# Kernel tuning notes

Measured on AMD Instinct MI355X. Metric: run time of the kernel, lower is better.

The kernel has to match this reference:

```python
import jax, jax.numpy as jnp
import numpy as np

B, T, N, E, H, L, K = 2, 32, 256, 1024, 16, 2, 256
MAXLEN = 512  # RelativeMultiheadAttention max_seq_len default
SCALES = (1, 2, 4)
TAU = 1.0


def setup_inputs() -> dict:
    key = jax.random.key(0)
    ks = jax.random.split(key, 9)
    s = 0.02
    A = 2 * L  # [layer0-spatial, layer0-temporal, layer1-spatial, layer1-temporal]
    return {
        "x": jax.random.normal(ks[0], (B, T, N, E), jnp.float32),
        "attn_wq": jax.random.normal(ks[1], (A, E, E), jnp.float32) * s,
        "attn_bq": jnp.zeros((A, E), jnp.float32),
        "attn_wk": jax.random.normal(ks[2], (A, E, E), jnp.float32) * s,
        "attn_bk": jnp.zeros((A, E), jnp.float32),
        "attn_wv": jax.random.normal(ks[3], (A, E, E), jnp.float32) * s,
        "attn_bv": jnp.zeros((A, E), jnp.float32),
        "attn_wd": jax.random.normal(ks[4], (A, E, E), jnp.float32) * s,
        "attn_bd": jnp.zeros((A, E), jnp.float32),
        "rel_bias": jax.random.normal(ks[5], (A, 2 * MAXLEN - 1, H), jnp.float32) * s,
        "sel_w": jax.random.normal(ks[6], (E, K), jnp.float32) * s,
        "sel_b": jnp.zeros((K,), jnp.float32),
    }


def _rel_attn(x, wq, bq, wk, bk, wv, bv, wd, bd, rb):
    # x: [Bx, S, E]; rb: [2*MAXLEN-1, H]
    Bx, S, _ = x.shape
    D = E // H
    q = (x @ wq + bq).reshape(Bx, S, H, D)
    k = (x @ wk + bk).reshape(Bx, S, H, D)
    v = (x @ wv + bv).reshape(Bx, S, H, D)
    scores = jnp.einsum('bshd,bthd->bhst', q, k) / jnp.sqrt(jnp.asarray(D, x.dtype))
    pos = jnp.arange(S)
    idx = pos[None, :] - pos[:, None] + (MAXLEN - 1)  # [S, S]
    bias = rb[idx]  # [S, S, H] gathered relative-position bias
    scores = scores + bias.transpose(2, 0, 1)[None]
    w = jax.nn.softmax(scores, axis=-1)
    ctx = jnp.einsum('bhst,bthd->bshd', w, v).reshape(Bx, S, E)
    return ctx @ wd + bd


def reference(x, attn_wq, attn_bq, attn_wk, attn_bk, attn_wv, attn_bv,
              attn_wd, attn_bd, rel_bias, sel_w, sel_b):
    h = x
    for l in range(L):
        # spatial attention over tokens within each frame
        i = 2 * l
        hs = h.reshape(B * T, N, E)
        hs = _rel_attn(hs, attn_wq[i], attn_bq[i], attn_wk[i], attn_bk[i],
                       attn_wv[i], attn_bv[i], attn_wd[i], attn_bd[i], rel_bias[i])
        # temporal attention across frames per spatial location
        j = 2 * l + 1
        ht = hs.reshape(B, T, N, E).transpose(0, 2, 1, 3).reshape(B * N, T, E)
        ht = _rel_attn(ht, attn_wq[j], attn_bq[j], attn_wk[j], attn_bk[j],
                       attn_wv[j], attn_bv[j], attn_wd[j], attn_bd[j], rel_bias[j])
        h = ht.reshape(B, N, T, E).transpose(0, 2, 1, 3)
    # DifferentiableTokenSelection: softmax-weighted pooling into K tokens
    flat = h.reshape(B, T * N, E)
    sc = flat @ sel_w + sel_b  # [B, T*N, K]
    wts = jax.nn.softmax(sc / TAU, axis=1)
    sel = jnp.einsum('bmk,bme->bke', wts, flat)  # [B, K, E]
    # multi-scale average pooling (kernel==stride==scale), concat along tokens
    outs = [sel.reshape(B, K // s, s, E).mean(axis=2) for s in SCALES]
    return jnp.concatenate(outs, axis=1)  # [B, K + K//2 + K//4, E]
```

## Files before the change

kernel.cpp:

```cpp
#include <hip/hip_runtime.h>
#include <stdint.h>


using f16x8 = __attribute__((ext_vector_type(8))) _Float16;
using f16x4 = __attribute__((ext_vector_type(4))) _Float16;
using f32x4 = __attribute__((ext_vector_type(4))) float;

__device__ __forceinline__ int tmap_dev(int m) {
    int bx = m >> 5;
    int s  = m & 31;
    int b  = bx >> 8;
    int n  = bx & 255;
    return (((b << 5) + s) << 8) + n;
}

__device__ __forceinline__ void load16(const _Float16* g, _Float16* l)
{
    __builtin_amdgcn_global_load_lds(
        (const __attribute__((address_space(1))) unsigned int*)g,
        (__attribute__((address_space(3))) unsigned int*)l,
        16, 0, 0);
}

__device__ __forceinline__ void split_f16(float v, _Float16& h, _Float16& l)
{
    h = (_Float16)v;
    l = (_Float16)(v - (float)h);
}

__global__ __launch_bounds__(256)
void conv_act(const float* __restrict__ src, _Float16* __restrict__ dh,
              _Float16* __restrict__ dl, int m_off)
{
    int idx = blockIdx.x * 256 + threadIdx.x;
    int e = idx << 3;
    int ml = e >> 10, col = e & 1023;
    const float* s = src + (size_t)(m_off + ml) * 1024 + col;
    float4 a = *(const float4*)s;
    float4 b = *(const float4*)(s + 4);
    float vv[8] = {a.x, a.y, a.z, a.w, b.x, b.y, b.z, b.w};
    f16x8 vh, vl;
    #pragma unroll
    for (int r = 0; r < 8; r++) {
        _Float16 h, l;
        split_f16(vv[r], h, l);
        vh[r] = h; vl[r] = l;
    }
    *(f16x8*)(dh + (size_t)ml * 1024 + col) = vh;
    *(f16x8*)(dl + (size_t)ml * 1024 + col) = vl;
}

__global__ __launch_bounds__(256)
void conv_wT(const float* __restrict__ W, _Float16* __restrict__ Th,
             _Float16* __restrict__ Tl, int ncols)
{
    __shared__ float Ls[64][65];
    const int n0 = blockIdx.x * 64, k0 = blockIdx.y * 64;
    const int t = threadIdx.x;
    const int kk = t >> 4, nn = (t & 15) << 2;
    #pragma unroll
    for (int i = 0; i < 4; i++) {
        float4 v = *(const float4*)(W + (size_t)(k0 + kk + 16 * i) * ncols + n0 + nn);
        Ls[kk + 16 * i][nn + 0] = v.x; Ls[kk + 16 * i][nn + 1] = v.y;
        Ls[kk + 16 * i][nn + 2] = v.z; Ls[kk + 16 * i][nn + 3] = v.w;
    }
    __syncthreads();
    const int nl = t >> 4, kc = (t & 15) << 2;
    #pragma unroll
    for (int i = 0; i < 4; i++) {
        int n = nl + 16 * i;
        f16x4 hh, ll;
        #pragma unroll
        for (int c = 0; c < 4; c++) {
            _Float16 h, l;
            split_f16(Ls[kc + c][n], h, l);
            hh[c] = h; ll[c] = l;
        }
        *(f16x4*)(Th + (size_t)(n0 + n) * 1024 + k0 + kc) = hh;
        *(f16x4*)(Tl + (size_t)(n0 + n) * 1024 + k0 + kc) = ll;
    }
}

template<int EPI>
__device__ __forceinline__ void gemm_core(
    const _Float16* __restrict__ Ah, const _Float16* __restrict__ Al,
    const _Float16* __restrict__ Wh, const _Float16* __restrict__ Wl,
    const float* __restrict__ bias,
    float* __restrict__ C, _Float16* __restrict__ Ch, _Float16* __restrict__ Cl,
    int ldc, int map_in, int m_off_in, int map_out, int m_off_out,
    int n0, int m0)
{
    __shared__ uint32_t smem_u[8512];
    _Float16* smem = (_Float16*)smem_u;
    _Float16* sAh = smem;
    _Float16* sAl = smem + 4096;
    _Float16* sBh = smem + 8192;
    _Float16* sBl = smem + 12288;

    const int tid = threadIdx.x;
    const int lane = tid & 63;
    const int wv = tid >> 6;
    const int fm = (wv >> 1) << 6;
    const int fn = (wv & 1) << 6;
    const int lm = lane & 15, lq = lane >> 4;

    f32x4 acc[4][4] = {};

    const int srow = tid >> 2;
    const int skc  = (tid & 3) << 3;
    const int gm0 = m_off_in + m0 + srow;
    const int gm1 = gm0 + 64;
    const int r0 = map_in ? tmap_dev(gm0) : gm0;
    const int r1 = map_in ? tmap_dev(gm1) : gm1;
    const _Float16* gAh0 = Ah + (size_t)r0 * 1024 + skc;
    const _Float16* gAh1 = Ah + (size_t)r1 * 1024 + skc;
    const _Float16* gAl0 = Al + (size_t)r0 * 1024 + skc;
    const _Float16* gAl1 = Al + (size_t)r1 * 1024 + skc;
    const _Float16* gB0 = Wh + (size_t)(n0 + srow) * 1024 + skc;
    const _Float16* gB1 = Wl + (size_t)(n0 + srow) * 1024 + skc;
    const int lo = tid << 3;

    for (int k0 = 0; k0 < 1024; k0 += 32) {
        load16(gAh0 + k0, sAh + lo);
        load16(gAh1 + k0, sAh + lo + 2048);
        load16(gAl0 + k0, sAl + lo);
        load16(gAl1 + k0, sAl + lo + 2048);
        load16(gB0 + k0,         sBh + lo);
        load16(gB0 + k0 + 65536, sBh + lo + 2048);
        load16(gB1 + k0,         sBl + lo);
        load16(gB1 + k0 + 65536, sBl + lo + 2048);
        __syncthreads();

        f16x8 ah[4], al[4], bh[4], bl[4];
        #pragma unroll
        for (int i = 0; i < 4; i++) {
            int ra = (fm + i * 16 + lm) * 32 + lq * 8;
            ah[i] = *(const f16x8*)(sAh + ra);
            al[i] = *(const f16x8*)(sAl + ra);
            int rb_ = (fn + i * 16 + lm) * 32 + lq * 8;
            bh[i] = *(const f16x8*)(sBh + rb_);
            bl[i] = *(const f16x8*)(sBl + rb_);
        }
        #pragma unroll
        for (int i = 0; i < 4; i++)
            #pragma unroll
            for (int j = 0; j < 4; j++) {
                acc[i][j] = __builtin_amdgcn_mfma_f32_16x16x32_f16(ah[i], bh[j], acc[i][j], 0, 0, 0);
                acc[i][j] = __builtin_amdgcn_mfma_f32_16x16x32_f16(ah[i], bl[j], acc[i][j], 0, 0, 0);
                acc[i][j] = __builtin_amdgcn_mfma_f32_16x16x32_f16(al[i], bh[j], acc[i][j], 0, 0, 0);
            }
        __syncthreads();
    }

    if (EPI == 0) {
        #pragma unroll
        for (int j = 0; j < 4; j++) {
            int n = n0 + fn + j * 16 + lm;
            float bb = bias[n];
            #pragma unroll
            for (int i = 0; i < 4; i++) {
                #pragma unroll
                for (int r = 0; r < 4; r++) {
                    int gm = m_off_out + m0 + fm + i * 16 + lq * 4 + r;
                    int row = map_out ? tmap_dev(gm) : gm;
                    C[(size_t)row * ldc + n] = acc[i][j][r] + bb;
                }
            }
        }
    }
}

__global__ __launch_bounds__(256, 2)
void gemm_f16s_f32(const _Float16* __restrict__ Ah, const _Float16* __restrict__ Al,
                   int map_in, int m_off_in,
                   const _Float16* __restrict__ Wh, const _Float16* __restrict__ Wl,
                   const float* __restrict__ bias, float* __restrict__ C, int ldc,
                   int map_out, int m_off_out)
{
    gemm_core<0>(Ah, Al, Wh, Wl, bias, C, nullptr, nullptr, ldc,
                 map_in, m_off_in, map_out, m_off_out,
                 blockIdx.x * 128, blockIdx.y * 128);
}

template<int EPI>
__device__ __forceinline__ void gemm256_core(
    uint32_t* __restrict__ smem_u,
    const _Float16* __restrict__ Ah, const _Float16* __restrict__ Al,
    const _Float16* __restrict__ Wh, const _Float16* __restrict__ Wl,
    const float* __restrict__ bias,
    _Float16* __restrict__ Ch, _Float16* __restrict__ Cl,
    int map_in, int m_off_in, int map_out, int m_off_out,
    int n0, int m0)
{
    _Float16* S = (_Float16*)smem_u;
    const int tid  = threadIdx.x;
    const int lane = tid & 63;
    const int wv = tid >> 6;
    const int wm = wv >> 1;
    const int fm = wm << 6;
    const int fn = (wv & 1) << 6;
    const int lm = lane & 15, lq = lane >> 4;
    const int ko = ((lq ^ ((lm >> 1) & 3)) << 3);

    f32x4 acc[4][4] = {};

    const int srow = tid >> 2;
    const int scol = (((tid & 3) ^ ((tid >> 3) & 3)) << 3);
    const int gm0 = m_off_in + m0 + srow;
    const int gm1 = gm0 + 128;
    const int r0 = map_in ? tmap_dev(gm0) : gm0;
    const int r1 = map_in ? tmap_dev(gm1) : gm1;
    const _Float16* gAh0 = Ah + (size_t)r0 * 1024 + scol;
    const _Float16* gAh1 = Ah + (size_t)r1 * 1024 + scol;
    const _Float16* gAl0 = Al + (size_t)r0 * 1024 + scol;
    const _Float16* gAl1 = Al + (size_t)r1 * 1024 + scol;
    const _Float16* gBh  = Wh + (size_t)(n0 + srow) * 1024 + scol;
    const _Float16* gBl  = Wl + (size_t)(n0 + srow) * 1024 + scol;
    const int lo = tid << 3;

    auto stage = [&](int t, int b) {
        const int k0 = t << 5;
        _Float16* d = S + b * 24576;
        load16(gAh0 + k0, d + lo);
        load16(gAh1 + k0, d + 4096  + lo);
        load16(gAl0 + k0, d + 8192  + lo);
        load16(gAl1 + k0, d + 12288 + lo);
        load16(gBh  + k0, d + 16384 + lo);
        load16(gBl  + k0, d + 20480 + lo);
    };

    auto ldfrags = [&](const _Float16* c,
                       f16x8 (&xah)[4], f16x8 (&xal)[4],
                       f16x8 (&xbh)[4], f16x8 (&xbl)[4]) {
        #pragma unroll
        for (int i = 0; i < 4; i++) {
            int ra = (fm + i * 16 + lm) * 32 + ko;
            xah[i] = *(const f16x8*)(c + ra);
            xal[i] = *(const f16x8*)(c + 8192 + ra);
            int rb = (fn + i * 16 + lm) * 32 + ko;
            xbh[i] = *(const f16x8*)(c + 16384 + rb);
            xbl[i] = *(const f16x8*)(c + 20480 + rb);
        }
    };

    f16x8 ahA[4], alA[4], bhA[4], blA[4];
    f16x8 ahB[4], alB[4], bhB[4], blB[4];

    auto kstep = [&](int t, int nxtbuf, int stagebuf,
                     f16x8 (&cah)[4], f16x8 (&cal)[4],
                     f16x8 (&cbh)[4], f16x8 (&cbl)[4],
                     f16x8 (&nah)[4], f16x8 (&nal)[4],
                     f16x8 (&nbh)[4], f16x8 (&nbl)[4],
                     bool prefetch, bool dostage) {
        if (prefetch) ldfrags(S + nxtbuf * 24576, nah, nal, nbh, nbl);
        if (dostage) stage(t + 2, stagebuf);
        __builtin_amdgcn_sched_barrier(0);
        __builtin_amdgcn_s_setprio(1);
        #pragma unroll
        for (int i = 0; i < 4; i++)
            #pragma unroll
            for (int j = 0; j < 4; j++) {
                acc[i][j] = __builtin_amdgcn_mfma_f32_16x16x32_f16(cah[i], cbh[j], acc[i][j], 0, 0, 0);
                acc[i][j] = __builtin_amdgcn_mfma_f32_16x16x32_f16(cah[i], cbl[j], acc[i][j], 0, 0, 0);
                acc[i][j] = __builtin_amdgcn_mfma_f32_16x16x32_f16(cal[i], cbh[j], acc[i][j], 0, 0, 0);
            }
        __builtin_amdgcn_s_setprio(0);
        asm volatile("s_waitcnt vmcnt(0)" ::: "memory");
        __builtin_amdgcn_s_barrier();
    };

    stage(0, 0);
    stage(1, 1);
    asm volatile("s_waitcnt vmcnt(0)" ::: "memory");
    __builtin_amdgcn_s_barrier();
    ldfrags(S, ahA, alA, bhA, blA);

    #pragma unroll 1
    for (int tt = 0; tt < 30; tt += 6) {
        kstep(tt + 0, 1, 2, ahA, alA, bhA, blA, ahB, alB, bhB, blB, true, true);
        kstep(tt + 1, 2, 0, ahB, alB, bhB, blB, ahA, alA, bhA, blA, true, true);
        kstep(tt + 2, 0, 1, ahA, alA, bhA, blA, ahB, alB, bhB, blB, true, true);
        kstep(tt + 3, 1, 2, ahB, alB, bhB, blB, ahA, alA, bhA, blA, true, true);
        kstep(tt + 4, 2, 0, ahA, alA, bhA, blA, ahB, alB, bhB, blB, true, true);
        kstep(tt + 5, 0, 1, ahB, alB, bhB, blB, ahA, alA, bhA, blA, true, true);
    }
    kstep(30, 1, 0, ahA, alA, bhA, blA, ahB, alB, bhB, blB, true,  false);
    kstep(31, 0, 0, ahB, alB, bhB, blB, ahA, alA, bhA, blA, false, false);

    if (EPI == 1) {
        #pragma unroll 1
        for (int q = 0; q < 4; q++) {
            __syncthreads();
            if (wm == q) {
                #pragma unroll
                for (int j = 0; j < 4; j++) {
                    int ncol = fn + j * 16 + lm;
                    float bb = bias[n0 + ncol];
                    #pragma unroll
                    for (int i = 0; i < 4; i++) {
                        #pragma unroll
                        for (int r = 0; r < 4; r++) {
                            float v = acc[i][j][r] + bb;
                            _Float16 h, l;
                            split_f16(v, h, l);
                            uint32_t ph = (uint32_t)__builtin_bit_cast(unsigned short, h);
                            uint32_t pl = (uint32_t)__builtin_bit_cast(unsigned short, l);
                            smem_u[(i * 16 + lq * 4 + r) * 132 + ncol] = ph | (pl << 16);
                        }
                    }
                }
            }
            __syncthreads();
            #pragma unroll
            for (int g = 0; g < 2; g++) {
                int u = tid + g * 512;
                int rl = u >> 4;
                int c8 = (u & 15) << 3;
                uint32_t p[8];
                #pragma unroll
                for (int x = 0; x < 8; x++) p[x] = smem_u[rl * 132 + c8 + x];
                f16x8 hh, ll;
                #pragma unroll
                for (int x = 0; x < 8; x++) {
                    hh[x] = __builtin_bit_cast(_Float16, (unsigned short)(p[x] & 0xffff));
                    ll[x] = __builtin_bit_cast(_Float16, (unsigned short)(p[x] >> 16));
                }
                int gm = m_off_out + m0 + q * 64 + rl;
                int row = map_out ? tmap_dev(gm) : gm;
                *(f16x8*)(Ch + (size_t)row * 1024 + n0 + c8) = hh;
                *(f16x8*)(Cl + (size_t)row * 1024 + n0 + c8) = ll;
            }
        }
    } else {
        #pragma unroll 1
        for (int q = 0; q < 4; q++) {
            __syncthreads();
            if (wm == q) {
                #pragma unroll
                for (int j = 0; j < 4; j++) {
                    int ncol = fn + j * 16 + lm;
                    float bb = bias[n0 + ncol];
                    #pragma unroll
                    for (int i = 0; i < 4; i++) {
                        #pragma unroll
                        for (int r = 0; r < 4; r++) {
                            float v = acc[i][j][r] + bb;
                            _Float16 h, l;
                            split_f16(v, h, l);
                            uint32_t ph = (uint32_t)__builtin_bit_cast(unsigned short, h);
                            uint32_t pl = (uint32_t)__builtin_bit_cast(unsigned short, l);
                            smem_u[(i * 16 + lq * 4 + r) * 129 + ncol] = ph | (pl << 16);
                        }
                    }
                }
            }
            __syncthreads();
            #pragma unroll
            for (int g = 0; g < 4; g++) {
                int u = tid + g * 512;
                int nn = u >> 4;
                int mg = (u & 15) << 2;
                uint32_t p0 = smem_u[(mg + 0) * 129 + nn];
                uint32_t p1 = smem_u[(mg + 1) * 129 + nn];
                uint32_t p2 = smem_u[(mg + 2) * 129 + nn];
                uint32_t p3 = smem_u[(mg + 3) * 129 + nn];
                f16x4 hh, ll;
                hh[0] = __builtin_bit_cast(_Float16, (unsigned short)(p0 & 0xffff));
                hh[1] = __builtin_bit_cast(_Float16, (unsigned short)(p1 & 0xffff));
                hh[2] = __builtin_bit_cast(_Float16, (unsigned short)(p2 & 0xffff));
                hh[3] = __builtin_bit_cast(_Float16, (unsigned short)(p3 & 0xffff));
                ll[0] = __builtin_bit_cast(_Float16, (unsigned short)(p0 >> 16));
                ll[1] = __builtin_bit_cast(_Float16, (unsigned short)(p1 >> 16));
                ll[2] = __builtin_bit_cast(_Float16, (unsigned short)(p2 >> 16));
                ll[3] = __builtin_bit_cast(_Float16, (unsigned short)(p3 >> 16));
                size_t off = (size_t)(n0 + nn) * 8192 + (m0 + q * 64 + mg);
                *(f16x4*)(Ch + off) = hh;
                *(f16x4*)(Cl + off) = ll;
            }
        }
    }
}

__global__ __launch_bounds__(512, 2)
void gemm_qkv256(const _Float16* __restrict__ Ah, const _Float16* __restrict__ Al,
                 int map_in, int m_off_in,
                 const _Float16* __restrict__ WTh, const _Float16* __restrict__ WTl,
                 const float* __restrict__ bq, const float* __restrict__ bk,
                 const float* __restrict__ bv,
                 _Float16* __restrict__ Qh, _Float16* __restrict__ Ql,
                 _Float16* __restrict__ Kh, _Float16* __restrict__ Kl,
                 _Float16* __restrict__ VTh, _Float16* __restrict__ VTl)
{
    __shared__ uint32_t smem_u[36864];
    const int bid = blockIdx.x;
    const int wg = (bid & 7) * 96 + (bid >> 3);
    const int z = wg >> 8;
    const int rem = wg & 255;
    const int m0 = (rem >> 3) << 8;
    const int n0 = (rem & 7) << 7;
    const _Float16* wh = WTh + (size_t)z * 1048576;
    const _Float16* wl = WTl + (size_t)z * 1048576;
    if (z < 2) {
        const float* bb = (z == 0) ? bq : bk;
        _Float16* oh = (z == 0) ? Qh : Kh;
        _Float16* ol = (z == 0) ? Ql : Kl;
        gemm256_core<1>(smem_u, Ah, Al, wh, wl, bb, oh, ol,
                        map_in, m_off_in, 0, 0, n0, m0);
    } else {
        gemm256_core<3>(smem_u, Ah, Al, wh, wl, bv, VTh, VTl,
                        map_in, m_off_in, 0, 0, n0, m0);
    }
}

__global__ __launch_bounds__(512, 2)
void gemm_h256(const _Float16* __restrict__ Ah, const _Float16* __restrict__ Al,
               int map_in, int m_off_in,
               const _Float16* __restrict__ Wh, const _Float16* __restrict__ Wl,
               const float* __restrict__ bias,
               _Float16* __restrict__ Ch, _Float16* __restrict__ Cl,
               int map_out, int m_off_out)
{
    __shared__ uint32_t smem_u[36864];
    const int bid = blockIdx.x;
    const int wg = (bid & 7) * 32 + (bid >> 3);
    const int m0 = (wg >> 3) << 8;
    const int n0 = (wg & 7) << 7;
    gemm256_core<1>(smem_u, Ah, Al, Wh, Wl, bias, Ch, Cl,
                    map_in, m_off_in, map_out, m_off_out, n0, m0);
}

__global__ __launch_bounds__(256, 2)
void attn_s_m(const _Float16* __restrict__ Qh, const _Float16* __restrict__ Ql,
              const _Float16* __restrict__ Kh, const _Float16* __restrict__ Kl,
              const _Float16* __restrict__ VTh, const _Float16* __restrict__ VTl,
              const float* __restrict__ RB,
              _Float16* __restrict__ Ch, _Float16* __restrict__ Cl)
{
    __shared__ _Float16 sKh[2048], sKl[2048];
    __shared__ _Float16 sVh[2560], sVl[2560];
    __shared__ _Float16 sPh[4][2560], sPl[4][2560];
    __shared__ float Bt[512];

    const int tid = threadIdx.x;
    const int lane = tid & 63;
    const int w = tid >> 6;
    const int lm = lane & 15, lq = lane >> 4;
    const int frame = blockIdx.x;
    const int h = blockIdx.y;
    const int rowbase = frame * 256;

    #pragma unroll
    for (int l = 0; l < 2; l++) {
        int idx = tid + l * 256;
        if (idx < 511) Bt[idx] = RB[(size_t)(256 + idx) * 16 + h];
    }

    f16x8 qbh[4][2], qbl[4][2];
    #pragma unroll
    for (int st = 0; st < 4; st++)
        #pragma unroll
        for (int kk = 0; kk < 2; kk++) {
            size_t qo = (size_t)(rowbase + w * 64 + st * 16 + lm) * 1024
                        + h * 64 + kk * 32 + lq * 8;
            qbh[st][kk] = *(const f16x8*)(Qh + qo);
            qbl[st][kk] = *(const f16x8*)(Ql + qo);
        }

    f32x4 cacc[4][4] = {};
    float lsum[4] = {0.f, 0.f, 0.f, 0.f};
    _Float16* Ph = sPh[w];
    _Float16* Pl = sPl[w];

    const int skrow = tid >> 3, skd = (tid & 7) << 3;
    const int svrow = tid >> 2, svj = (tid & 3) << 3;

    for (int jc = 0; jc < 8; jc++) {
        __syncthreads();
        {
            size_t ko = (size_t)(rowbase + jc * 32 + skrow) * 1024 + h * 64 + skd;
            *(f16x8*)(sKh + skrow * 64 + skd) = *(const f16x8*)(Kh + ko);
            *(f16x8*)(sKl + skrow * 64 + skd) = *(const f16x8*)(Kl + ko);
            size_t vo = (size_t)(h * 64 + svrow) * 8192 + rowbase + jc * 32 + svj;
            *(f16x8*)(sVh + svrow * 40 + svj) = *(const f16x8*)(VTh + vo);
            *(f16x8*)(sVl + svrow * 40 + svj) = *(const f16x8*)(VTl + vo);
        }
        __syncthreads();

        f32x4 sacc[2][4] = {};
        #pragma unroll
        for (int jt = 0; jt < 2; jt++) {
            f16x8 kah[2], kal[2];
            #pragma unroll
            for (int kk = 0; kk < 2; kk++) {
                int ra = (jt * 16 + lm) * 64 + kk * 32 + lq * 8;
                kah[kk] = *(const f16x8*)(sKh + ra);
                kal[kk] = *(const f16x8*)(sKl + ra);
            }
            #pragma unroll
            for (int st = 0; st < 4; st++)
                #pragma unroll
                for (int kk = 0; kk < 2; kk++) {
                    sacc[jt][st] = __builtin_amdgcn_mfma_f32_16x16x32_f16(kah[kk], qbh[st][kk], sacc[jt][st], 0, 0, 0);
                    sacc[jt][st] = __builtin_amdgcn_mfma_f32_16x16x32_f16(kah[kk], qbl[st][kk], sacc[jt][st], 0, 0, 0);
                    sacc[jt][st] = __builtin_amdgcn_mfma_f32_16x16x32_f16(kal[kk], qbh[st][kk], sacc[jt][st], 0, 0, 0);
                }
        }

        #pragma unroll
        for (int jt = 0; jt < 2; jt++)
            #pragma unroll
            for (int st = 0; st < 4; st++) {
                f16x4 p4h, p4l;
                #pragma unroll
                for (int r = 0; r < 4; r++) {
                    int j = jc * 32 + jt * 16 + lq * 4 + r;
                    int s = w * 64 + st * 16 + lm;
                    float p = __expf(sacc[jt][st][r] * 0.125f + Bt[j - s + 255]);
                    lsum[st] += p;
                    _Float16 hp, lp;
                    split_f16(p, hp, lp);
                    p4h[r] = hp; p4l[r] = lp;
                }
                int pa = (st * 16 + lm) * 40 + jt * 16 + lq * 4;
                *(f16x4*)(Ph + pa) = p4h;
                *(f16x4*)(Pl + pa) = p4l;
            }

        #pragma unroll
        for (int st = 0; st < 4; st++) {
            int pb = (st * 16 + lm) * 40 + lq * 8;
            f16x8 pbh = *(const f16x8*)(Ph + pb);
            f16x8 pbl = *(const f16x8*)(Pl + pb);
            #pragma unroll
            for (int dt = 0; dt < 4; dt++) {
                int va = (dt * 16 + lm) * 40 + lq * 8;
                f16x8 vah = *(const f16x8*)(sVh + va);
                f16x8 val = *(const f16x8*)(sVl + va);
                cacc[dt][st] = __builtin_amdgcn_mfma_f32_16x16x32_f16(vah, pbh, cacc[dt][st], 0, 0, 0);
                cacc[dt][st] = __builtin_amdgcn_mfma_f32_16x16x32_f16(vah, pbl, cacc[dt][st], 0, 0, 0);
                cacc[dt][st] = __builtin_amdgcn_mfma_f32_16x16x32_f16(val, pbh, cacc[dt][st], 0, 0, 0);
            }
        }
    }

    float inv[4];
    #pragma unroll
    for (int st = 0; st < 4; st++) {
        float t = lsum[st];
        t += __shfl_xor(t, 16);
        t += __shfl_xor(t, 32);
        inv[st] = 1.0f / t;
    }

    #pragma unroll
    for (int st = 0; st < 4; st++)
        #pragma unroll
        for (int dt = 0; dt < 4; dt++) {
            f16x4 oh, ol;
            #pragma unroll
            for (int r = 0; r < 4; r++) {
                _Float16 hp, lp;
                split_f16(cacc[dt][st][r] * inv[st], hp, lp);
                oh[r] = hp; ol[r] = lp;
            }
            size_t oo = (size_t)(rowbase + w * 64 + st * 16 + lm) * 1024
                        + h * 64 + dt * 16 + lq * 4;
            *(f16x4*)(Ch + oo) = oh;
            *(f16x4*)(Cl + oo) = ol;
        }
}

__global__ __launch_bounds__(256, 2)
void attn_t_m(const _Float16* __restrict__ Qh, const _Float16* __restrict__ Ql,
              const _Float16* __restrict__ Kh, const _Float16* __restrict__ Kl,
              const _Float16* __restrict__ VTh, const _Float16* __restrict__ VTl,
              const float* __restrict__ RB,
              _Float16* __restrict__ Ch, _Float16* __restrict__ Cl)
{
    __shared__ _Float16 sPh[4][1280], sPl[4][1280];
    __shared__ float Bt[64];

    const int tid = threadIdx.x;
    const int lane = tid & 63;
    const int w = tid >> 6;
    const int lm = lane & 15, lq = lane >> 4;
    const int h = blockIdx.y;
    const int bx = blockIdx.x * 4 + w;
    const int rowbase = bx * 32;

    if (tid < 63) Bt[tid] = RB[(size_t)(480 + tid) * 16 + h];
    __syncthreads();

    f16x8 qbh[2][2], qbl[2][2];
    #pragma unroll
    for (int st = 0; st < 2; st++)
        #pragma unroll
        for (int kk = 0; kk < 2; kk++) {
            size_t qo = (size_t)(rowbase + st * 16 + lm) * 1024 + h * 64 + kk * 32 + lq * 8;
            qbh[st][kk] = *(const f16x8*)(Qh + qo);
            qbl[st][kk] = *(const f16x8*)(Ql + qo);
        }

    f32x4 sacc[2][2] = {};
    #pragma unroll
    for (int jt = 0; jt < 2; jt++) {
        f16x8 kah[2], kal[2];
        #pragma unroll
        for (int kk = 0; kk < 2; kk++) {
            size_t ko = (size_t)(rowbase + jt * 16 + lm) * 1024 + h * 64 + kk * 32 + lq * 8;
            kah[kk] = *(const f16x8*)(Kh + ko);
            kal[kk] = *(const f16x8*)(Kl + ko);
        }
        #pragma unroll
        for (int st = 0; st < 2; st++)
            #pragma unroll
            for (int kk = 0; kk < 2; kk++) {
                sacc[jt][st] = __builtin_amdgcn_mfma_f32_16x16x32_f16(kah[kk], qbh[st][kk], sacc[jt][st], 0, 0, 0);
                sacc[jt][st] = __builtin_amdgcn_mfma_f32_16x16x32_f16(kah[kk], qbl[st][kk], sacc[jt][st], 0, 0, 0);
                sacc[jt][st] = __builtin_amdgcn_mfma_f32_16x16x32_f16(kal[kk], qbh[st][kk], sacc[jt][st], 0, 0, 0);
            }
    }

    float lsum[2] = {0.f, 0.f};
    _Float16* Ph = sPh[w];
    _Float16* Pl = sPl[w];
    #pragma unroll
    for (int jt = 0; jt < 2; jt++)
        #pragma unroll
        for (int st = 0; st < 2; st++) {
            f16x4 p4h, p4l;
            #pragma unroll
            for (int r = 0; r < 4; r++) {
                int j = jt * 16 + lq * 4 + r;
                int s = st * 16 + lm;
                float p = __expf(sacc[jt][st][r] * 0.125f + Bt[j - s + 31]);
                lsum[st] += p;
                _Float16 hp, lp;
                split_f16(p, hp, lp);
                p4h[r] = hp; p4l[r] = lp;
            }
            int pa = (st * 16 + lm) * 40 + jt * 16 + lq * 4;
            *(f16x4*)(Ph + pa) = p4h;
            *(f16x4*)(Pl + pa) = p4l;
        }

    f16x8 vah[4], val[4];
    #pragma unroll
    for (int dt = 0; dt < 4; dt++) {
        size_t vo = (size_t)(h * 64 + dt * 16 + lm) * 8192 + rowbase + lq * 8;
        vah[dt] = *(const f16x8*)(VTh + vo);
        val[dt] = *(const f16x8*)(VTl + vo);
    }
    f32x4 cacc[4][2] = {};
    #pragma unroll
    for (int st = 0; st < 2; st++) {
        int pb = (st * 16 + lm) * 40 + lq * 8;
        f16x8 pbh = *(const f16x8*)(Ph + pb);
        f16x8 pbl = *(const f16x8*)(Pl + pb);
        #pragma unroll
        for (int dt = 0; dt < 4; dt++) {
            cacc[dt][st] = __builtin_amdgcn_mfma_f32_16x16x32_f16(vah[dt], pbh, cacc[dt][st], 0, 0, 0);
            cacc[dt][st] = __builtin_amdgcn_mfma_f32_16x16x32_f16(vah[dt], pbl, cacc[dt][st], 0, 0, 0);
            cacc[dt][st] = __builtin_amdgcn_mfma_f32_16x16x32_f16(val[dt], pbh, cacc[dt][st], 0, 0, 0);
        }
    }

    float inv[2];
    #pragma unroll
    for (int st = 0; st < 2; st++) {
        float t = lsum[st];
        t += __shfl_xor(t, 16);
        t += __shfl_xor(t, 32);
        inv[st] = 1.0f / t;
    }

    #pragma unroll
    for (int st = 0; st < 2; st++)
        #pragma unroll
        for (int dt = 0; dt < 4; dt++) {
            f16x4 oh, ol;
            #pragma unroll
            for (int r = 0; r < 4; r++) {
                _Float16 hp, lp;
                split_f16(cacc[dt][st][r] * inv[st], hp, lp);
                oh[r] = hp; ol[r] = lp;
            }
            size_t oo = (size_t)(rowbase + st * 16 + lm) * 1024 + h * 64 + dt * 16 + lq * 4;
            *(f16x4*)(Ch + oo) = oh;
            *(f16x4*)(Cl + oo) = ol;
        }
}

__global__ __launch_bounds__(256)
void colsum_part_kernel(const float* __restrict__ SC, float* __restrict__ P)
{
    int bid = blockIdx.x;
    int b = bid >> 7, chunk = bid & 127;
    int base = b * 8192 + chunk * 64;
    int k = threadIdx.x;
    float sum = 0.0f;
    for (int r = 0; r < 64; r++)
        sum += __expf(SC[(size_t)(base + r) * 256 + k]);
    P[(size_t)bid * 256 + k] = sum;
}

__global__ __launch_bounds__(256)
void colsum_reduce_kernel(const float* __restrict__ P, float* __restrict__ CS)
{
    int b = blockIdx.x;
    int k = threadIdx.x;
    float s = 0.0f;
    for (int c = 0; c < 128; c++)
        s += P[(size_t)(b * 128 + c) * 256 + k];
    CS[b * 256 + k] = s;
}

__global__ __launch_bounds__(256)
void trans_wts(const float* __restrict__ SC, const float* __restrict__ CS,
               _Float16* __restrict__ Th, _Float16* __restrict__ Tl)
{
    __shared__ float L[64][65];
    const int mt = blockIdx.x * 64;
    const int kt = blockIdx.y * 64;
    const int b  = mt >> 13;
    const int ml = mt & 8191;
    const int tid = threadIdx.x;
    #pragma unroll
    for (int l = 0; l < 4; l++) {
        int idx = tid + 256 * l;
        int r = idx >> 4, c4 = (idx & 15) << 2;
        float4 v = *(const float4*)(SC + (size_t)(mt + r) * 256 + kt + c4);
        L[r][c4 + 0] = __expf(v.x); L[r][c4 + 1] = __expf(v.y);
        L[r][c4 + 2] = __expf(v.z); L[r][c4 + 3] = __expf(v.w);
    }
    __syncthreads();
    #pragma unroll
    for (int l = 0; l < 4; l++) {
        int idx = tid + 256 * l;
        int rk = idx >> 4, c4 = (idx & 15) << 2;
        float inv = 1.0f / CS[b * 256 + kt + rk];
        f16x4 hh, ll;
        #pragma unroll
        for (int u = 0; u < 4; u++) {
            _Float16 h, l2;
            split_f16(L[c4 + u][rk] * inv, h, l2);
            hh[u] = h; ll[u] = l2;
        }
        size_t o = ((size_t)b * 256 + kt + rk) * 8192 + ml + c4;
        *(f16x4*)(Th + o) = hh;
        *(f16x4*)(Tl + o) = ll;
    }
}

__global__ __launch_bounds__(256)
void trans_f16(const _Float16* __restrict__ Sh, const _Float16* __restrict__ Sl,
               _Float16* __restrict__ Th, _Float16* __restrict__ Tl)
{
    __shared__ _Float16 L[64][72];
    const int mt = blockIdx.x * 64, et = blockIdx.y * 64;
    const _Float16* S = blockIdx.z ? Sl : Sh;
    _Float16* T = blockIdx.z ? Tl : Th;
    const int tid = threadIdx.x;
    #pragma unroll
    for (int l = 0; l < 2; l++) {
        int v = tid * 2 + l;
        int r = v >> 3, c8 = (v & 7) << 3;
        *(f16x8*)&L[r][c8] = *(const f16x8*)(S + (size_t)(mt + r) * 1024 + et + c8);
    }
    __syncthreads();
    #pragma unroll
    for (int l = 0; l < 2; l++) {
        int v = tid * 2 + l;
        int r = v >> 3, c8 = (v & 7) << 3;
        f16x8 o;
        #pragma unroll
        for (int u = 0; u < 8; u++) o[u] = L[c8 + u][r];
        *(f16x8*)(T + (size_t)(et + r) * 16384 + mt + c8) = o;
    }
}

__global__ __launch_bounds__(256, 2)
void gemm_selm(const _Float16* __restrict__ Wth, const _Float16* __restrict__ Wtl,
               const _Float16* __restrict__ Hth, const _Float16* __restrict__ Htl,
               float* __restrict__ P)
{
    __shared__ _Float16 sAh[4096], sAl[4096], sBh[4096], sBl[4096];
    const int tid = threadIdx.x;
    const int lane = tid & 63;
    const int wv = tid >> 6;
    const int fm = (wv >> 1) << 6;
    const int fn = (wv & 1) << 6;
    const int lm = lane & 15, lq = lane >> 4;
    const int n0 = blockIdx.x * 128;
    const int m0 = blockIdx.y * 128;
    const int z  = blockIdx.z;
    const int b = z >> 3, sp = z & 7;

    f32x4 acc[4][4] = {};

    const int srow = tid >> 2;
    const int skc  = (tid & 3) << 3;
    const _Float16* gAh0 = Wth + ((size_t)b * 256 + m0 + srow) * 8192 + sp * 1024 + skc;
    const _Float16* gAl0 = Wtl + ((size_t)b * 256 + m0 + srow) * 8192 + sp * 1024 + skc;
    const _Float16* gB0 = Hth + (size_t)(n0 + srow) * 16384 + b * 8192 + sp * 1024 + skc;
    const _Float16* gB1 = Htl + (size_t)(n0 + srow) * 16384 + b * 8192 + sp * 1024 + skc;
    const int lo = tid << 3;

    for (int k0 = 0; k0 < 1024; k0 += 32) {
        load16(gAh0 + k0,          sAh + lo);
        load16(gAh0 + k0 + 524288, sAh + lo + 2048);
        load16(gAl0 + k0,          sAl + lo);
        load16(gAl0 + k0 + 524288, sAl + lo + 2048);
        load16(gB0 + k0,           sBh + lo);
        load16(gB0 + k0 + 1048576, sBh + lo + 2048);
        load16(gB1 + k0,           sBl + lo);
        load16(gB1 + k0 + 1048576, sBl + lo + 2048);
        __syncthreads();

        f16x8 ah[4], al[4], bh[4], bl[4];
        #pragma unroll
        for (int i = 0; i < 4; i++) {
            int ra = (fm + i * 16 + lm) * 32 + lq * 8;
            ah[i] = *(const f16x8*)(sAh + ra);
            al[i] = *(const f16x8*)(sAl + ra);
            int rb_ = (fn + i * 16 + lm) * 32 + lq * 8;
            bh[i] = *(const f16x8*)(sBh + rb_);
            bl[i] = *(const f16x8*)(sBl + rb_);
        }
        #pragma unroll
        for (int i = 0; i < 4; i++)
            #pragma unroll
            for (int j = 0; j < 4; j++) {
                acc[i][j] = __builtin_amdgcn_mfma_f32_16x16x32_f16(ah[i], bh[j], acc[i][j], 0, 0, 0);
                acc[i][j] = __builtin_amdgcn_mfma_f32_16x16x32_f16(ah[i], bl[j], acc[i][j], 0, 0, 0);
                acc[i][j] = __builtin_amdgcn_mfma_f32_16x16x32_f16(al[i], bh[j], acc[i][j], 0, 0, 0);
            }
        __syncthreads();
    }

    float* Pz = P + (size_t)z * 262144;
    #pragma unroll
    for (int j = 0; j < 4; j++) {
        int n = n0 + fn + j * 16 + lm;
        #pragma unroll
        for (int i = 0; i < 4; i++)
            #pragma unroll
            for (int r = 0; r < 4; r++) {
                int k = m0 + fm + i * 16 + lq * 4 + r;
                Pz[(size_t)k * 1024 + n] = acc[i][j][r];
            }
    }
}

__global__ __launch_bounds__(256)
void sel_reduce(const float* __restrict__ P, float* __restrict__ SEL)
{
    int idx4 = blockIdx.x * 256 + threadIdx.x;
    int e = idx4 << 2;
    int b = e >> 18;
    int rest = e & 262143;
    const float* p = P + (size_t)(b * 8) * 262144 + rest;
    float4 acc = {0.f, 0.f, 0.f, 0.f};
    #pragma unroll
    for (int s = 0; s < 8; s++) {
        float4 v = *(const float4*)(p + (size_t)s * 262144);
        acc.x += v.x; acc.y += v.y; acc.z += v.z; acc.w += v.w;
    }
    *(float4*)(SEL + e) = acc;
}

__global__ __launch_bounds__(256)
void pool_kernel(const float* __restrict__ SEL, float* __restrict__ out)
{
    int i4 = blockIdx.x * 256 + threadIdx.x;
    int e  = i4 << 2;
    int row = e >> 10;
    int b = row / 448;
    int r = row - b * 448;
    int c = e & 1023;
    const float* sb = SEL + (size_t)b * (256 * 1024);
    float4 o;
    if (r < 256) {
        o = *(const float4*)(sb + (size_t)r * 1024 + c);
    } else if (r < 384) {
        int r2 = (r - 256) * 2;
        float4 x0 = *(const float4*)(sb + (size_t)r2 * 1024 + c);
        float4 x1 = *(const float4*)(sb + (size_t)(r2 + 1) * 1024 + c);
        o.x = 0.5f * (x0.x + x1.x); o.y = 0.5f * (x0.y + x1.y);
        o.z = 0.5f * (x0.z + x1.z); o.w = 0.5f * (x0.w + x1.w);
    } else {
        int r4 = (r - 384) * 4;
        float4 x0 = *(const float4*)(sb + (size_t)(r4 + 0) * 1024 + c);
        float4 x1 = *(const float4*)(sb + (size_t)(r4 + 1) * 1024 + c);
        float4 x2 = *(const float4*)(sb + (size_t)(r4 + 2) * 1024 + c);
        float4 x3 = *(const float4*)(sb + (size_t)(r4 + 3) * 1024 + c);
        o.x = 0.25f * (x0.x + x1.x + x2.x + x3.x);
        o.y = 0.25f * (x0.y + x1.y + x2.y + x3.y);
        o.z = 0.25f * (x0.z + x1.z + x2.z + x3.z);
        o.w = 0.25f * (x0.w + x1.w + x2.w + x3.w);
    }
    *(float4*)(out + e) = o;
}

extern "C" void kernel_launch(void* const* d_in, const int* in_sizes, int n_in,
                              void* d_out, int out_size, void* d_ws, size_t ws_size,
                              hipStream_t stream)
{
    const float* x    = (const float*)d_in[0];
    const float* wq   = (const float*)d_in[1];
    const float* bq   = (const float*)d_in[2];
    const float* wk   = (const float*)d_in[3];
    const float* bk   = (const float*)d_in[4];
    const float* wv   = (const float*)d_in[5];
    const float* bv   = (const float*)d_in[6];
    const float* wd   = (const float*)d_in[7];
    const float* bd   = (const float*)d_in[8];
    const float* rb   = (const float*)d_in[9];
    const float* selw = (const float*)d_in[10];
    const float* selb = (const float*)d_in[11];
    float* out = (float*)d_out;

    float* base = (float*)d_ws;
    _Float16* Hh  = (_Float16*)base;
    _Float16* Hl  = Hh + 16777216;
    _Float16* Qh  = (_Float16*)(base + 16777216);
    _Float16* Ql  = Qh + 8388608;
    _Float16* Kh  = Ql + 8388608;
    _Float16* Kl  = Kh + 8388608;
    _Float16* VTh = (_Float16*)(base + 33554432);
    _Float16* VTl = VTh + 8388608;
    _Float16* CXh = (_Float16*)(base + 41943040);
    _Float16* CXl = CXh + 8388608;
    _Float16* WTh = (_Float16*)(base + 50331648);
    _Float16* WTl = WTh + 4194304;
    _Float16* Ah  = (_Float16*)(base + 54525952);
    _Float16* Al  = Ah + 8388608;
    float* SC   = (float*)Qh;
    float* Pp   = (float*)Kh;
    float* SEL  = (float*)Kl;
    float* PART = SEL + 524288;
    float* CSUM = PART + 65536;
    _Float16* WTTh = CXh;
    _Float16* WTTl = CXl;
    _Float16* HTh  = Ah;
    _Float16* HTl  = VTh;

    const dim3 blk(256);
    const dim3 blk2(512);

    for (int a = 0; a < 4; a++) {
        const int mi = (a & 1);
        const size_t wo = (size_t)a * 1048576;
        const int bo = a * 1024;
        const float* rba = rb + (size_t)a * 1023 * 16;

        conv_wT<<<dim3(16, 16), blk, 0, stream>>>(wq + wo, WTh,           WTl,           1024);
        conv_wT<<<dim3(16, 16), blk, 0, stream>>>(wk + wo, WTh + 1048576, WTl + 1048576, 1024);
        conv_wT<<<dim3(16, 16), blk, 0, stream>>>(wv + wo, WTh + 2097152, WTl + 2097152, 1024);
        conv_wT<<<dim3(16, 16), blk, 0, stream>>>(wd + wo, WTh + 3145728, WTl + 3145728, 1024);

        for (int c = 0; c < 2; c++) {
            const int mo = c * 8192;
            const _Float16 *sH, *sL;
            int sm, so;
            if (a == 0) {
                conv_act<<<4096, blk, 0, stream>>>(x, Ah, Al, mo);
                sH = Ah; sL = Al; sm = 0; so = 0;
            } else {
                sH = Hh; sL = Hl; sm = mi; so = mo;
            }
            gemm_qkv256<<<dim3(768), blk2, 0, stream>>>(
                sH, sL, sm, so, WTh, WTl, bq + bo, bk + bo, bv + bo,
                Qh, Ql, Kh, Kl, VTh, VTl);
            if (mi == 0)
                attn_s_m<<<dim3(32, 16), blk, 0, stream>>>(Qh, Ql, Kh, Kl, VTh, VTl, rba, CXh, CXl);
            else
                attn_t_m<<<dim3(64, 16), blk, 0, stream>>>(Qh, Ql, Kh, Kl, VTh, VTl, rba, CXh, CXl);
            gemm_h256<<<dim3(256), blk2, 0, stream>>>(
                CXh, CXl, 0, 0, WTh + 3145728, WTl + 3145728, bd + bo, Hh, Hl, mi, mo);
        }
    }

    conv_wT<<<dim3(4, 16), blk, 0, stream>>>(selw, WTh, WTl, 256);
    gemm_f16s_f32<<<dim3(2, 128), blk, 0, stream>>>(
        Hh, Hl, 0, 0, WTh, WTl, selb, SC, 256, 0, 0);
    colsum_part_kernel<<<256, blk, 0, stream>>>(SC, PART);
    colsum_reduce_kernel<<<2, blk, 0, stream>>>(PART, CSUM);
    trans_wts<<<dim3(256, 4), blk, 0, stream>>>(SC, CSUM, WTTh, WTTl);
    trans_f16<<<dim3(256, 16, 2), blk, 0, stream>>>(Hh, Hl, HTh, HTl);
    gemm_selm<<<dim3(8, 2, 16), blk, 0, stream>>>(WTTh, WTTl, HTh, HTl, Pp);
    sel_reduce<<<512, blk, 0, stream>>>(Pp, SEL);
    pool_kernel<<<896, blk, 0, stream>>>(SEL, out);
}
```

Measured before the change: 2.515 ms.

## Interleave LDS fragment reads and split global staging between MFMA groups

Reworks the 256-row GEMM main loop so each k-step reads A fragments one row-group at a time and prefetches next-step B fragments in pieces. These reads are interleaved with groups of MFMAs. The global-to-LDS staging is split into three parts spread across the step, so memory issue overlaps with compute. This replaces the fully double-buffered A/B register fragments, which cuts VGPR pressure under the 512-thread launch bound. It also drops the explicit sched_barrier and setprio hints and the barrier after the last steps, which leaves more scheduling to the compiler.

```diff
diff --git a/kernel.cpp b/kernel.cpp
--- a/kernel.cpp
+++ b/kernel.cpp
@@ -182,6 +182,47 @@
                  blockIdx.x * 128, blockIdx.y * 128);
 }
 
+#define RD_A(DH, DL, BASE, II)                                                   \
+    DH = *(const f16x8*)((BASE) + (fm + (II) * 16 + lm) * 32 + ko);              \
+    DL = *(const f16x8*)((BASE) + 8192 + (fm + (II) * 16 + lm) * 32 + ko);
+
+#define RD_B(BH, BL, BASE, JJ)                                                   \
+    BH[JJ] = *(const f16x8*)((BASE) + 16384 + (fn + (JJ) * 16 + lm) * 32 + ko);  \
+    BL[JJ] = *(const f16x8*)((BASE) + 20480 + (fn + (JJ) * 16 + lm) * 32 + ko);
+
+#define MM1(AH, AL, BH, BL, II, JJ)                                                         \
+    acc[II][JJ] = __builtin_amdgcn_mfma_f32_16x16x32_f16(AH, BH[JJ], acc[II][JJ], 0, 0, 0); \
+    acc[II][JJ] = __builtin_amdgcn_mfma_f32_16x16x32_f16(AH, BL[JJ], acc[II][JJ], 0, 0, 0); \
+    acc[II][JJ] = __builtin_amdgcn_mfma_f32_16x16x32_f16(AL, BH[JJ], acc[II][JJ], 0, 0, 0);
+
+#define MMG(AH, AL, BH, BL, II)                                                  \
+    MM1(AH, AL, BH, BL, II, 0) MM1(AH, AL, BH, BL, II, 1)                        \
+    MM1(AH, AL, BH, BL, II, 2) MM1(AH, AL, BH, BL, II, 3)
+
+#define KSTEP(T, CUR, NXT, STG, BHc, BLc, BHn, BLn, DOSTAGE, DONEXT, DOSYNC)     \
+{                                                                                \
+    const _Float16* cbuf = S + (CUR) * 24576;                                    \
+    const _Float16* nbuf = S + (NXT) * 24576;                                    \
+    RD_A(a1h, a1l, cbuf, 1)                                                      \
+    if (DONEXT) { RD_B(BHn, BLn, nbuf, 0) RD_B(BHn, BLn, nbuf, 1) }              \
+    if (DOSTAGE) stage_part((T) + 2, (STG), 0);                                  \
+    MMG(a0h, a0l, BHc, BLc, 0)                                                   \
+    RD_A(a0h, a0l, cbuf, 2)                                                      \
+    if (DONEXT) { RD_B(BHn, BLn, nbuf, 2) }                                      \
+    if (DOSTAGE) stage_part((T) + 2, (STG), 1);                                  \
+    MMG(a1h, a1l, BHc, BLc, 1)                                                   \
+    RD_A(a1h, a1l, cbuf, 3)                                                      \
+    if (DONEXT) { RD_B(BHn, BLn, nbuf, 3) }                                      \
+    if (DOSTAGE) stage_part((T) + 2, (STG), 2);                                  \
+    MMG(a0h, a0l, BHc, BLc, 2)                                                   \
+    if (DONEXT) { RD_A(a0h, a0l, nbuf, 0) }                                      \
+    MMG(a1h, a1l, BHc, BLc, 3)                                                   \
+    if (DOSYNC) {                                                                \
+        asm volatile("s_waitcnt vmcnt(0)" ::: "memory");                         \
+        __builtin_amdgcn_s_barrier();                                            \
+    }                                                                            \
+}
+
 template<int EPI>
 __device__ __forceinline__ void gemm256_core(
     uint32_t* __restrict__ smem_u,
@@ -218,74 +259,43 @@
     const _Float16* gBl  = Wl + (size_t)(n0 + srow) * 1024 + scol;
     const int lo = tid << 3;
 
-    auto stage = [&](int t, int b) {
+    auto stage_part = [&](int t, int b, int part) {
         const int k0 = t << 5;
         _Float16* d = S + b * 24576;
-        load16(gAh0 + k0, d + lo);
-        load16(gAh1 + k0, d + 4096  + lo);
-        load16(gAl0 + k0, d + 8192  + lo);
-        load16(gAl1 + k0, d + 12288 + lo);
-        load16(gBh  + k0, d + 16384 + lo);
-        load16(gBl  + k0, d + 20480 + lo);
+        if (part == 0) {
+            load16(gAh0 + k0, d + lo);
+            load16(gAh1 + k0, d + 4096  + lo);
+        } else if (part == 1) {
+            load16(gAl0 + k0, d + 8192  + lo);
+            load16(gAl1 + k0, d + 12288 + lo);
+        } else {
+            load16(gBh  + k0, d + 16384 + lo);
+            load16(gBl  + k0, d + 20480 + lo);
+        }
     };
 
-    auto ldfrags = [&](const _Float16* c,
-                       f16x8 (&xah)[4], f16x8 (&xal)[4],
-                       f16x8 (&xbh)[4], f16x8 (&xbl)[4]) {
-        #pragma unroll
-        for (int i = 0; i < 4; i++) {
-            int ra = (fm + i * 16 + lm) * 32 + ko;
-            xah[i] = *(const f16x8*)(c + ra);
-            xal[i] = *(const f16x8*)(c + 8192 + ra);
-            int rb = (fn + i * 16 + lm) * 32 + ko;
-            xbh[i] = *(const f16x8*)(c + 16384 + rb);
-            xbl[i] = *(const f16x8*)(c + 20480 + rb);
-        }
-    };
-
-    f16x8 ahA[4], alA[4], bhA[4], blA[4];
-    f16x8 ahB[4], alB[4], bhB[4], blB[4];
-
-    auto kstep = [&](int t, int nxtbuf, int stagebuf,
-                     f16x8 (&cah)[4], f16x8 (&cal)[4],
-                     f16x8 (&cbh)[4], f16x8 (&cbl)[4],
-                     f16x8 (&nah)[4], f16x8 (&nal)[4],
-                     f16x8 (&nbh)[4], f16x8 (&nbl)[4],
-                     bool prefetch, bool dostage) {
-        if (prefetch) ldfrags(S + nxtbuf * 24576, nah, nal, nbh, nbl);
-        if (dostage) stage(t + 2, stagebuf);
-        __builtin_amdgcn_sched_barrier(0);
-        __builtin_amdgcn_s_setprio(1);
-        #pragma unroll
-        for (int i = 0; i < 4; i++)
-            #pragma unroll
-            for (int j = 0; j < 4; j++) {
-                acc[i][j] = __builtin_amdgcn_mfma_f32_16x16x32_f16(cah[i], cbh[j], acc[i][j], 0, 0, 0);
-                acc[i][j] = __builtin_amdgcn_mfma_f32_16x16x32_f16(cah[i], cbl[j], acc[i][j], 0, 0, 0);
-                acc[i][j] = __builtin_amdgcn_mfma_f32_16x16x32_f16(cal[i], cbh[j], acc[i][j], 0, 0, 0);
-            }
-        __builtin_amdgcn_s_setprio(0);
-        asm volatile("s_waitcnt vmcnt(0)" ::: "memory");
-        __builtin_amdgcn_s_barrier();
-    };
-
-    stage(0, 0);
-    stage(1, 1);
+    f16x8 bh0[4], bl0[4], bh1[4], bl1[4];
+    f16x8 a0h, a0l, a1h, a1l;
+
+    stage_part(0, 0, 0); stage_part(0, 0, 1); stage_part(0, 0, 2);
+    stage_part(1, 1, 0); stage_part(1, 1, 1); stage_part(1, 1, 2);
     asm volatile("s_waitcnt vmcnt(0)" ::: "memory");
     __builtin_amdgcn_s_barrier();
-    ldfrags(S, ahA, alA, bhA, blA);
+    RD_B(bh0, bl0, S, 0) RD_B(bh0, bl0, S, 1)
+    RD_B(bh0, bl0, S, 2) RD_B(bh0, bl0, S, 3)
+    RD_A(a0h, a0l, S, 0)
 
     #pragma unroll 1
     for (int tt = 0; tt < 30; tt += 6) {
-        kstep(tt + 0, 1, 2, ahA, alA, bhA, blA, ahB, alB, bhB, blB, true, true);
-        kstep(tt + 1, 2, 0, ahB, alB, bhB, blB, ahA, alA, bhA, blA, true, true);
-        kstep(tt + 2, 0, 1, ahA, alA, bhA, blA, ahB, alB, bhB, blB, true, true);
-        kstep(tt + 3, 1, 2, ahB, alB, bhB, blB, ahA, alA, bhA, blA, true, true);
-        kstep(tt + 4, 2, 0, ahA, alA, bhA, blA, ahB, alB, bhB, blB, true, true);
-        kstep(tt + 5, 0, 1, ahB, alB, bhB, blB, ahA, alA, bhA, blA, true, true);
-    }
-    kstep(30, 1, 0, ahA, alA, bhA, blA, ahB, alB, bhB, blB, true,  false);
-    kstep(31, 0, 0, ahB, alB, bhB, blB, ahA, alA, bhA, blA, false, false);
+        KSTEP(tt + 0, 0, 1, 2, bh0, bl0, bh1, bl1, true, true, true)
+        KSTEP(tt + 1, 1, 2, 0, bh1, bl1, bh0, bl0, true, true, true)
+        KSTEP(tt + 2, 2, 0, 1, bh0, bl0, bh1, bl1, true, true, true)
+        KSTEP(tt + 3, 0, 1, 2, bh1, bl1, bh0, bl0, true, true, true)
+        KSTEP(tt + 4, 1, 2, 0, bh0, bl0, bh1, bl1, true, true, true)
+        KSTEP(tt + 5, 2, 0, 1, bh1, bl1, bh0, bl0, true, true, true)
+    }
+    KSTEP(30, 0, 1, 2, bh0, bl0, bh1, bl1, false, true, false)
+    KSTEP(31, 1, 2, 0, bh1, bl1, bh0, bl0, false, false, false)
 
     if (EPI == 1) {
         #pragma unroll 1
@@ -380,6 +390,12 @@
         }
     }
 }
+
+#undef RD_A
+#undef RD_B
+#undef MM1
+#undef MMG
+#undef KSTEP
 
 __global__ __launch_bounds__(512, 2)
 void gemm_qkv256(const _Float16* __restrict__ Ah, const _Float16* __restrict__ Al,
```

Measured after the change: 2.319 ms. 1.08x faster.

## Replace register-prefetch GEMM pipeline with partial vmcnt waits on triple-buffered LDS

Applied to the files above, without the earlier changes.

The 256-tile fp16-split GEMM main loop no longer double-buffers LDS fragments in registers across k-steps. Each step now waits only until the older global-to-LDS loads have landed (vmcnt(6)) and syncs on a barrier. It then issues the next stage, reads fragments and runs the MFMAs. This keeps the newest prefetch in flight instead of draining all loads every step, and frees the second fragment register set. The trade-off is that LDS fragment reads are no longer overlapped with the previous step's MFMAs. Unused epilogue parameters are also removed from the 128-tile GEMM helper.

```diff
diff --git a/kernel.cpp b/kernel.cpp
--- a/kernel.cpp
+++ b/kernel.cpp
@@ -86,16 +86,11 @@
     const _Float16* __restrict__ Ah, const _Float16* __restrict__ Al,
     const _Float16* __restrict__ Wh, const _Float16* __restrict__ Wl,
     const float* __restrict__ bias,
-    float* __restrict__ C, _Float16* __restrict__ Ch, _Float16* __restrict__ Cl,
-    int ldc, int map_in, int m_off_in, int map_out, int m_off_out,
+    float* __restrict__ C, int ldc,
+    int map_in, int m_off_in, int map_out, int m_off_out,
     int n0, int m0)
 {
-    __shared__ uint32_t smem_u[8512];
-    _Float16* smem = (_Float16*)smem_u;
-    _Float16* sAh = smem;
-    _Float16* sAl = smem + 4096;
-    _Float16* sBh = smem + 8192;
-    _Float16* sBl = smem + 12288;
+    __shared__ _Float16 sAh[4096], sAl[4096], sBh[4096], sBl[4096];
 
     const int tid = threadIdx.x;
     const int lane = tid & 63;
@@ -177,7 +172,7 @@
                    const float* __restrict__ bias, float* __restrict__ C, int ldc,
                    int map_out, int m_off_out)
 {
-    gemm_core<0>(Ah, Al, Wh, Wl, bias, C, nullptr, nullptr, ldc,
+    gemm_core<0>(Ah, Al, Wh, Wl, bias, C, ldc,
                  map_in, m_off_in, map_out, m_off_out,
                  blockIdx.x * 128, blockIdx.y * 128);
 }
@@ -222,70 +217,52 @@
         const int k0 = t << 5;
         _Float16* d = S + b * 24576;
         load16(gAh0 + k0, d + lo);
-        load16(gAh1 + k0, d + 4096  + lo);
+        load16(gAh1 + k0, d + 2048 * 2 + lo);
         load16(gAl0 + k0, d + 8192  + lo);
         load16(gAl1 + k0, d + 12288 + lo);
         load16(gBh  + k0, d + 16384 + lo);
         load16(gBl  + k0, d + 20480 + lo);
     };
 
-    auto ldfrags = [&](const _Float16* c,
-                       f16x8 (&xah)[4], f16x8 (&xal)[4],
-                       f16x8 (&xbh)[4], f16x8 (&xbl)[4]) {
+    auto kstep = [&](int t, int cb, int sb, bool last) {
+        if (last) asm volatile("s_waitcnt vmcnt(0) lgkmcnt(0)" ::: "memory");
+        else      asm volatile("s_waitcnt vmcnt(6) lgkmcnt(0)" ::: "memory");
+        __builtin_amdgcn_s_barrier();
+        if (sb >= 0) stage(t + 2, sb);
+
+        const _Float16* c = S + cb * 24576;
+        f16x8 ah[4], al[4], bh[4], bl[4];
         #pragma unroll
         for (int i = 0; i < 4; i++) {
             int ra = (fm + i * 16 + lm) * 32 + ko;
-            xah[i] = *(const f16x8*)(c + ra);
-            xal[i] = *(const f16x8*)(c + 8192 + ra);
+            ah[i] = *(const f16x8*)(c + ra);
+            al[i] = *(const f16x8*)(c + 8192 + ra);
             int rb = (fn + i * 16 + lm) * 32 + ko;
-            xbh[i] = *(const f16x8*)(c + 16384 + rb);
-            xbl[i] = *(const f16x8*)(c + 20480 + rb);
-        }
-    };
-
-    f16x8 ahA[4], alA[4], bhA[4], blA[4];
-    f16x8 ahB[4], alB[4], bhB[4], blB[4];
-
-    auto kstep = [&](int t, int nxtbuf, int stagebuf,
-                     f16x8 (&cah)[4], f16x8 (&cal)[4],
-                     f16x8 (&cbh)[4], f16x8 (&cbl)[4],
-                     f16x8 (&nah)[4], f16x8 (&nal)[4],
-                     f16x8 (&nbh)[4], f16x8 (&nbl)[4],
-                     bool prefetch, bool dostage) {
-        if (prefetch) ldfrags(S + nxtbuf * 24576, nah, nal, nbh, nbl);
-        if (dostage) stage(t + 2, stagebuf);
-        __builtin_amdgcn_sched_barrier(0);
+            bh[i] = *(const f16x8*)(c + 16384 + rb);
+            bl[i] = *(const f16x8*)(c + 20480 + rb);
+        }
         __builtin_amdgcn_s_setprio(1);
         #pragma unroll
         for (int i = 0; i < 4; i++)
             #pragma unroll
             for (int j = 0; j < 4; j++) {
-                acc[i][j] = __builtin_amdgcn_mfma_f32_16x16x32_f16(cah[i], cbh[j], acc[i][j], 0, 0, 0);
-                acc[i][j] = __builtin_amdgcn_mfma_f32_16x16x32_f16(cah[i], cbl[j], acc[i][j], 0, 0, 0);
-                acc[i][j] = __builtin_amdgcn_mfma_f32_16x16x32_f16(cal[i], cbh[j], acc[i][j], 0, 0, 0);
+                acc[i][j] = __builtin_amdgcn_mfma_f32_16x16x32_f16(ah[i], bh[j], acc[i][j], 0, 0, 0);
+                acc[i][j] = __builtin_amdgcn_mfma_f32_16x16x32_f16(ah[i], bl[j], acc[i][j], 0, 0, 0);
+                acc[i][j] = __builtin_amdgcn_mfma_f32_16x16x32_f16(al[i], bh[j], acc[i][j], 0, 0, 0);
             }
         __builtin_amdgcn_s_setprio(0);
-        asm volatile("s_waitcnt vmcnt(0)" ::: "memory");
-        __builtin_amdgcn_s_barrier();
     };
 
     stage(0, 0);
     stage(1, 1);
-    asm volatile("s_waitcnt vmcnt(0)" ::: "memory");
-    __builtin_amdgcn_s_barrier();
-    ldfrags(S, ahA, alA, bhA, blA);
-
     #pragma unroll 1
-    for (int tt = 0; tt < 30; tt += 6) {
-        kstep(tt + 0, 1, 2, ahA, alA, bhA, blA, ahB, alB, bhB, blB, true, true);
-        kstep(tt + 1, 2, 0, ahB, alB, bhB, blB, ahA, alA, bhA, blA, true, true);
-        kstep(tt + 2, 0, 1, ahA, alA, bhA, blA, ahB, alB, bhB, blB, true, true);
-        kstep(tt + 3, 1, 2, ahB, alB, bhB, blB, ahA, alA, bhA, blA, true, true);
-        kstep(tt + 4, 2, 0, ahA, alA, bhA, blA, ahB, alB, bhB, blB, true, true);
-        kstep(tt + 5, 0, 1, ahB, alB, bhB, blB, ahA, alA, bhA, blA, true, true);
-    }
-    kstep(30, 1, 0, ahA, alA, bhA, blA, ahB, alB, bhB, blB, true,  false);
-    kstep(31, 0, 0, ahB, alB, bhB, blB, ahA, alA, bhA, blA, false, false);
+    for (int tt = 0; tt < 30; tt += 3) {
+        kstep(tt + 0, 0, 2, false);
+        kstep(tt + 1, 1, 0, false);
+        kstep(tt + 2, 2, 1, false);
+    }
+    kstep(30, 0, -1, false);
+    kstep(31, 1, -1, true);
 
     if (EPI == 1) {
         #pragma unroll 1
```

Result: faster. 2.205 ms (-12.3%).
